# Kernel optimization log

Measured on AMD Instinct MI355X. Metric: run time of the kernel, lower is better.

The kernel has to match this reference:

```python
import jax, jax.numpy as jnp
import numpy as np

N, E = 50000, 640000
IN, HD, OUT, NCLS = 768, 128, 128, 2
H, C = 4, 32  # heads, per-head channels (HD/H = OUT/H = 32)
NEG_SLOPE = 0.2


def _glorot(key, shape):
    fan_in, fan_out = shape[0], shape[1]
    lim = jnp.sqrt(6.0 / (fan_in + fan_out))
    return jax.random.uniform(key, shape, jnp.float32, -lim, lim)


def setup_inputs() -> dict:
    key = jax.random.key(0)
    ks = jax.random.split(key, 24)
    x = jax.random.normal(ks[0], (1, N, IN), jnp.float32)
    edge_index = jax.random.randint(ks[1], (2, E), 0, N, jnp.int64)
    d = {"x": x, "edge_index": edge_index}
    ins = [IN, HD, HD, HD]
    for i in range(4):
        d[f"Wl{i+1}"] = _glorot(ks[2 + 5 * i], (ins[i], H * C))
        d[f"Wr{i+1}"] = _glorot(ks[3 + 5 * i], (ins[i], H * C))
        d[f"att{i+1}"] = _glorot(ks[4 + 5 * i], (H, C))
        d[f"b{i+1}"] = jnp.zeros((H * C,), jnp.float32)
    d["clfW"] = _glorot(ks[22], (OUT, NCLS))
    d["clfb"] = jnp.zeros((NCLS,), jnp.float32)
    return d


def _gatv2_layer(x, Wl, Wr, att, b, src, dst):
    # x: [N, F_in] -> out: [N, H*C]. GATv2: e = a^T LeakyReLU(xl_j + xr_i)
    xl = (x @ Wl).reshape(N, H, C)
    xr = (x @ Wr).reshape(N, H, C)
    h = xl[src] + xr[dst]                                   # [E', H, C] per-edge gather
    e = jnp.einsum('ehc,hc->eh', jax.nn.leaky_relu(h, NEG_SLOPE), att)
    m = jax.ops.segment_max(e, dst, num_segments=N)          # scatter-softmax (stable)
    a = jnp.exp(e - m[dst])
    s = jax.ops.segment_sum(a, dst, num_segments=N)
    alpha = a / (s[dst] + 1e-16)
    out = jax.ops.segment_sum(alpha[..., None] * xl[src], dst, num_segments=N)
    return out.reshape(N, H * C) + b


def reference(x, edge_index, Wl1, Wr1, att1, b1, Wl2, Wr2, att2, b2,
              Wl3, Wr3, att3, b3, Wl4, Wr4, att4, b4, clfW, clfb):
    xn = x.reshape(N, IN)  # torch.squeeze
    loops = jnp.arange(N, dtype=edge_index.dtype)  # PyG add_self_loops=True
    src = jnp.concatenate([edge_index[0], loops])
    dst = jnp.concatenate([edge_index[1], loops])
    h = jax.nn.relu(_gatv2_layer(xn, Wl1, Wr1, att1, b1, src, dst))
    h = jax.nn.relu(_gatv2_layer(h, Wl2, Wr2, att2, b2, src, dst))
    h = jax.nn.relu(_gatv2_layer(h, Wl3, Wr3, att3, b3, src, dst))
    h = _gatv2_layer(h, Wl4, Wr4, att4, b4, src, dst)        # [N, OUT]
    g = jnp.mean(h, axis=0, keepdims=True)                   # unsqueeze+mean over nodes -> [1, OUT]
    return g @ clfW + clfb                                   # [1, NCLS]
```

## Files before the change

kernel.cpp:

```cpp
#include <hip/hip_runtime.h>
#include <hip/hip_bf16.h>

#define NN 50000
#define EE 640000
#define HC 128
#define NB1 196

typedef short bf16x8 __attribute__((ext_vector_type(8)));
typedef float f32x4 __attribute__((ext_vector_type(4)));
typedef unsigned short u16;

__device__ __forceinline__ u16 f2b(float f) {
    unsigned u = __float_as_uint(f);
    unsigned r = u + 0x7FFFu + ((u >> 16) & 1u);
    return (u16)(r >> 16);
}
__device__ __forceinline__ float b2f(u16 h) {
    return __uint_as_float(((unsigned)h) << 16);
}

__device__ __forceinline__ void gload_lds16(const void* g, void* l) {
    __builtin_amdgcn_global_load_lds((const __attribute__((address_space(1))) void*)g,
                                     (__attribute__((address_space(3))) void*)l, 16, 0, 0);
}

__device__ __forceinline__ float red16(float x) {
    x += __int_as_float(__builtin_amdgcn_update_dpp(0, __float_as_int(x), 0xB1, 0xF, 0xF, true));
    x += __int_as_float(__builtin_amdgcn_update_dpp(0, __float_as_int(x), 0x4E, 0xF, 0xF, true));
    x += __int_as_float(__builtin_amdgcn_update_dpp(0, __float_as_int(x), 0x141, 0xF, 0xF, true));
    x += __int_as_float(__builtin_amdgcn_update_dpp(0, __float_as_int(x), 0x128, 0xF, 0xF, true));
    return x;
}


__global__ void k_count(const int* __restrict__ ei, int* __restrict__ cnt) {
    int e = blockIdx.x * blockDim.x + threadIdx.x;
    if (e < EE) atomicAdd(&cnt[ei[EE + e]], 1);
}

__global__ void k_bsum(const int* __restrict__ cnt, int* __restrict__ bsum) {
    __shared__ int sd[256];
    int b = blockIdx.x, t = threadIdx.x, i = b * 256 + t;
    sd[t] = (i < NN) ? cnt[i] + 1 : 0;
    __syncthreads();
    for (int o = 128; o; o >>= 1) { if (t < o) sd[t] += sd[t + o]; __syncthreads(); }
    if (!t) bsum[b] = sd[0];
}

__global__ void k_offs(const int* __restrict__ cnt_in, const int* __restrict__ bsum,
                       int* __restrict__ offs, int* __restrict__ cursor,
                       int* __restrict__ csr) {
    __shared__ int sb[256];
    __shared__ int sd[256];
    int b = blockIdx.x, t = threadIdx.x, i = b * 256 + t;
    sb[t] = (t < NB1) ? bsum[t] : 0;
    int v = (i < NN) ? cnt_in[i] + 1 : 0;
    sd[t] = v;
    __syncthreads();
    for (int o = 1; o < 256; o <<= 1) {
        int u1 = (t >= o) ? sd[t - o] : 0;
        int u2 = (t >= o) ? sb[t - o] : 0;
        __syncthreads();
        sd[t] += u1; sb[t] += u2;
        __syncthreads();
    }
    int bex = (b > 0) ? sb[b - 1] : 0;
    if (i < NN) {
        int o = bex + sd[t] - v;
        offs[i] = o;
        csr[o] = i;
        cursor[i] = o + 1;
    }
    if (b == NB1 - 1 && t == 0) offs[NN] = sb[NB1 - 1];
}

__global__ void k_fill(const int* __restrict__ ei, int* __restrict__ cursor,
                       int* __restrict__ csr) {
    int e = blockIdx.x * blockDim.x + threadIdx.x;
    if (e < EE) {
        int s = ei[e], d = ei[EE + e];
        int pos = atomicAdd(&cursor[d], 1);
        csr[pos] = s;
    }
}


#define WT_L0 196608
#define WT_LX 32768
#define WT_TOT (WT_L0 + 3 * WT_LX)

__global__ void k_castw_all(const float* __restrict__ Wl1, const float* __restrict__ Wr1,
                            const float* __restrict__ Wl2, const float* __restrict__ Wr2,
                            const float* __restrict__ Wl3, const float* __restrict__ Wr3,
                            const float* __restrict__ Wl4, const float* __restrict__ Wr4,
                            u16* __restrict__ WtAll) {
    int gid = blockIdx.x * 256 + threadIdx.x;
    if (gid >= WT_TOT) return;
    const float *Wl, *Wr;
    int idx, K, base;
    if (gid < WT_L0) { Wl = Wl1; Wr = Wr1; idx = gid; K = 768; base = 0; }
    else {
        int r = gid - WT_L0;
        int l = r >> 15; idx = r & (WT_LX - 1); K = 128; base = WT_L0 + l * WT_LX;
        if (l == 0)      { Wl = Wl2; Wr = Wr2; }
        else if (l == 1) { Wl = Wl3; Wr = Wr3; }
        else             { Wl = Wl4; Wr = Wr4; }
    }
    int c = idx / K, k = idx - c * K;
    float v = (c < 128) ? Wl[k * 128 + c] : Wr[k * 128 + (c - 128)];
    WtAll[base + idx] = f2b(v);
}


template<int K, bool F32A>
__global__ __launch_bounds__(512, 4)
void k_gemm(const void* __restrict__ Ag, const u16* __restrict__ Wt,
            u16* __restrict__ xb) {
    __shared__ __align__(16) u16 As[128 * 64];
    __shared__ __align__(16) u16 Bs[256 * 64];
    const int tid = threadIdx.x;
    const int wv = tid >> 6, ln = tid & 63;
    const int wr = wv >> 2, wc = wv & 3;
    const int m0 = blockIdx.x * 128;
    const int lrow = ln & 15, g = ln >> 4;

    f32x4 acc[4][4] = {};

    const float* Af = (const float*)Ag;
    const u16* Ab = (const u16*)Ag;
    const int arow = tid >> 2, aq = tid & 3;
    int arg = m0 + arow; if (arg >= NN) arg = 0;
    float4 ra0, ra1, ra2, ra3;

    if constexpr (F32A) {
        const float* src = Af + (size_t)arg * K + aq * 16;
        ra0 = *(const float4*)(src);
        ra1 = *(const float4*)(src + 4);
        ra2 = *(const float4*)(src + 8);
        ra3 = *(const float4*)(src + 12);
    }

    constexpr int NSTEP = K / 64;
    for (int ks = 0; ks < NSTEP; ++ks) {
        if constexpr (F32A) {
            const int s = arow & 7;
            bf16x8 v0, v1;
            v0[0] = (short)f2b(ra0.x); v0[1] = (short)f2b(ra0.y);
            v0[2] = (short)f2b(ra0.z); v0[3] = (short)f2b(ra0.w);
            v0[4] = (short)f2b(ra1.x); v0[5] = (short)f2b(ra1.y);
            v0[6] = (short)f2b(ra1.z); v0[7] = (short)f2b(ra1.w);
            v1[0] = (short)f2b(ra2.x); v1[1] = (short)f2b(ra2.y);
            v1[2] = (short)f2b(ra2.z); v1[3] = (short)f2b(ra2.w);
            v1[4] = (short)f2b(ra3.x); v1[5] = (short)f2b(ra3.y);
            v1[6] = (short)f2b(ra3.z); v1[7] = (short)f2b(ra3.w);
            *(bf16x8*)&As[arow * 64 + (((aq * 2) ^ s) * 8)] = v0;
            *(bf16x8*)&As[arow * 64 + (((aq * 2 + 1) ^ s) * 8)] = v1;
        } else {
            #pragma unroll
            for (int q = 0; q < 2; ++q) {
                int r8 = (wv * 2 + q) * 8;
                int row = r8 + (ln >> 3);
                int lc = (ln & 7) ^ (row & 7);
                int rg = m0 + row; if (rg >= NN) rg = 0;
                gload_lds16(Ab + (size_t)rg * K + ks * 64 + lc * 8, &As[r8 * 64]);
            }
        }
        #pragma unroll
        for (int q = 0; q < 4; ++q) {
            int r8 = (wv * 4 + q) * 8;
            int row = r8 + (ln >> 3);
            int lc = (ln & 7) ^ (row & 7);
            gload_lds16(Wt + (size_t)row * K + ks * 64 + lc * 8, &Bs[r8 * 64]);
        }
        __syncthreads();

        if constexpr (F32A) {
            if (ks + 1 < NSTEP) {
                const float* src = Af + (size_t)arg * K + (ks + 1) * 64 + aq * 16;
                ra0 = *(const float4*)(src);
                ra1 = *(const float4*)(src + 4);
                ra2 = *(const float4*)(src + 8);
                ra3 = *(const float4*)(src + 12);
            }
        }

        #pragma unroll
        for (int kk = 0; kk < 2; ++kk) {
            bf16x8 af[4], bfr[4];
            #pragma unroll
            for (int f = 0; f < 4; ++f) {
                int r = wr * 64 + f * 16 + lrow;
                af[f] = *(const bf16x8*)&As[r * 64 + (((kk * 4 + g) ^ (r & 7)) * 8)];
                int c = wc * 64 + f * 16 + lrow;
                bfr[f] = *(const bf16x8*)&Bs[c * 64 + (((kk * 4 + g) ^ (c & 7)) * 8)];
            }
            #pragma unroll
            for (int i = 0; i < 4; ++i)
                #pragma unroll
                for (int j = 0; j < 4; ++j)
                    acc[i][j] = __builtin_amdgcn_mfma_f32_16x16x32_bf16(af[i], bfr[j], acc[i][j], 0, 0, 0);
        }
        __syncthreads();
    }

    const int crow0 = m0 + wr * 64 + (g << 2);
    const int ccol0 = wc * 64 + lrow;
    #pragma unroll
    for (int i = 0; i < 4; ++i)
        #pragma unroll
        for (int rr = 0; rr < 4; ++rr) {
            int row = crow0 + i * 16 + rr;
            if (row < NN) {
                #pragma unroll
                for (int j = 0; j < 4; ++j)
                    xb[(size_t)row * 256 + ccol0 + j * 16] = f2b(acc[i][j][rr]);
            }
        }
}


__global__ __launch_bounds__(256)
void k_edge(const u16* __restrict__ xb, const float* __restrict__ att,
            const float* __restrict__ bias, const int* __restrict__ offs,
            const int* __restrict__ csr, u16* __restrict__ outb,
            float* __restrict__ outf, int relu) {
    int i = blockIdx.x * 4 + (threadIdx.x >> 6);
    if (i >= NN) return;
    int ln = threadIdx.x & 63;
    int ch0 = ((ln >> 4) << 5) + ((ln & 15) << 1);

    unsigned xr2 = *(const unsigned*)&xb[(size_t)i * 256 + 128 + ch0];
    float xri0 = b2f((u16)xr2), xri1 = b2f((u16)(xr2 >> 16));
    float2 atv = *(const float2*)&att[ch0];
    const float at0 = atv.x, at1 = atv.y;
    int beg = offs[i];
    int deg = offs[i + 1] - beg;

    float m0v = -3.0e38f, s0v = 0.f, p00 = 0.f, p01 = 0.f;
    float m1v = -3.0e38f, s1v = 0.f, p10 = 0.f, p11 = 0.f;
    float m2v = -3.0e38f, s2v = 0.f, p20 = 0.f, p21 = 0.f;
    float m3v = -3.0e38f, s3v = 0.f, p30 = 0.f, p31 = 0.f;

#define GATH(k, jj) unsigned w##k = *(const unsigned*)&xb[(size_t)(jj) * 256 + ch0];
#define UPD(k, M, S, A0, A1) { \
    float v0 = b2f((u16)w##k), v1 = b2f((u16)(w##k >> 16)); \
    float u0 = v0 + xri0; u0 = fmaxf(u0, 0.2f * u0); \
    float u1 = v1 + xri1; u1 = fmaxf(u1, 0.2f * u1); \
    float e = red16(u0 * at0 + u1 * at1); \
    float d = e - M; \
    float tt = __expf(-fabsf(d)); \
    bool ng = (d <= 0.f); \
    float c = ng ? 1.f : tt; \
    float ww = ng ? tt : 1.f; \
    M = ng ? M : e; \
    S = S * c + ww; A0 = A0 * c + ww * v0; A1 = A1 * c + ww * v1; }

    for (int base = 0; base < deg; base += 64) {
        int lim = deg - base; if (lim > 64) lim = 64;
        int idxv = (base + ln < deg) ? csr[beg + base + ln] : 0;
        int p = 0;
        for (; p + 4 <= lim; p += 4) {
            int j0 = __shfl(idxv, p);
            int j1 = __shfl(idxv, p + 1);
            int j2 = __shfl(idxv, p + 2);
            int j3 = __shfl(idxv, p + 3);
            GATH(0, j0) GATH(1, j1) GATH(2, j2) GATH(3, j3)
            UPD(0, m0v, s0v, p00, p01)
            UPD(1, m1v, s1v, p10, p11)
            UPD(2, m2v, s2v, p20, p21)
            UPD(3, m3v, s3v, p30, p31)
        }
        for (; p < lim; ++p) {
            int j0 = __shfl(idxv, p);
            GATH(4, j0)
            UPD(4, m0v, s0v, p00, p01)
        }
    }
#undef GATH
#undef UPD

    float mm = fmaxf(fmaxf(m0v, m1v), fmaxf(m2v, m3v));
    float c0 = __expf(m0v - mm), c1 = __expf(m1v - mm);
    float c2 = __expf(m2v - mm), c3 = __expf(m3v - mm);
    float s = s0v * c0 + s1v * c1 + s2v * c2 + s3v * c3 + 1e-16f;
    float inv = 1.f / s;
    float2 bv = *(const float2*)&bias[ch0];
    float o0 = (p00 * c0 + p10 * c1 + p20 * c2 + p30 * c3) * inv + bv.x;
    float o1 = (p01 * c0 + p11 * c1 + p21 * c2 + p31 * c3) * inv + bv.y;
    if (relu) { o0 = fmaxf(o0, 0.f); o1 = fmaxf(o1, 0.f); }
    if (outb) {
        unsigned pk = (unsigned)f2b(o0) | ((unsigned)f2b(o1) << 16);
        *(unsigned*)&outb[(size_t)i * HC + ch0] = pk;
    }
    if (outf) {
        *(float2*)&outf[(size_t)i * HC + ch0] = make_float2(o0, o1);
    }
}


__global__ __launch_bounds__(256)
void k_colsum(const float* __restrict__ h, float* __restrict__ gsum) {
    __shared__ float4 sd[8][32];
    int t = threadIdx.x;
    int c4 = t & 31, rl = t >> 5;
    float sx = 0.f, sy = 0.f, sz = 0.f, sw = 0.f;
    for (int r = blockIdx.x * 8 + rl; r < NN; r += 8 * gridDim.x) {
        float4 v = *(const float4*)&h[(size_t)r * HC + c4 * 4];
        sx += v.x; sy += v.y; sz += v.z; sw += v.w;
    }
    sd[rl][c4] = make_float4(sx, sy, sz, sw);
    __syncthreads();
    if (rl == 0) {
        float4 a = sd[0][c4];
        #pragma unroll
        for (int q = 1; q < 8; ++q) {
            float4 b = sd[q][c4];
            a.x += b.x; a.y += b.y; a.z += b.z; a.w += b.w;
        }
        atomicAdd(&gsum[c4 * 4 + 0], a.x);
        atomicAdd(&gsum[c4 * 4 + 1], a.y);
        atomicAdd(&gsum[c4 * 4 + 2], a.z);
        atomicAdd(&gsum[c4 * 4 + 3], a.w);
    }
}

__global__ void k_clf(const float* __restrict__ gsum, const float* __restrict__ W,
                      const float* __restrict__ bcls, float* __restrict__ out) {
    __shared__ float v[HC];
    int t = threadIdx.x;
    v[t] = gsum[t] * (1.f / (float)NN);
    __syncthreads();
    if (t < 2) {
        float r = 0.f;
        for (int k = 0; k < HC; ++k) r += v[k] * W[k * 2 + t];
        out[t] = r + bcls[t];
    }
}


extern "C" void kernel_launch(void* const* d_in, const int* in_sizes, int n_in,
                              void* d_out, int out_size, void* d_ws, size_t ws_size,
                              hipStream_t stream) {
    const float* x = (const float*)d_in[0];
    const int* ei = (const int*)d_in[1];
    const float *Wl[4], *Wr[4], *att[4], *bia[4];
    for (int l = 0; l < 4; ++l) {
        Wl[l] = (const float*)d_in[2 + 4 * l];
        Wr[l] = (const float*)d_in[3 + 4 * l];
        att[l] = (const float*)d_in[4 + 4 * l];
        bia[l] = (const float*)d_in[5 + 4 * l];
    }
    const float* clfW = (const float*)d_in[18];
    const float* clfb = (const float*)d_in[19];
    float* outp = (float*)d_out;

    char* w = (char*)d_ws;
    size_t o = 0;
    auto alloc = [&](size_t bytes) {
        char* p = w + o;
        o = (o + bytes + 255) & ~(size_t)255;
        return p;
    };
    int* cnt    = (int*)alloc((size_t)NN * 4);
    float* gsum = (float*)alloc(HC * 4);
    size_t zspan = o;
    int* offs  = (int*)alloc((size_t)(NN + 1) * 4);
    int* csr   = (int*)alloc((size_t)(EE + NN) * 4);
    int* bsum  = (int*)alloc((size_t)NB1 * 4);
    u16* WtAll = (u16*)alloc((size_t)WT_TOT * 2);
    u16* xb    = (u16*)alloc((size_t)NN * 256 * 2);
    u16* hb0   = (u16*)alloc((size_t)NN * HC * 2);
    u16* hb1   = (u16*)alloc((size_t)NN * HC * 2);
    float* hfin = (float*)alloc((size_t)NN * HC * 4);

    hipMemsetAsync(cnt, 0, zspan, stream);
    k_count<<<(EE + 255) / 256, 256, 0, stream>>>(ei, cnt);
    k_bsum<<<NB1, 256, 0, stream>>>(cnt, bsum);
    k_offs<<<NB1, 256, 0, stream>>>(cnt, bsum, offs, cnt, csr);
    k_fill<<<(EE + 255) / 256, 256, 0, stream>>>(ei, cnt, csr);
    k_castw_all<<<(WT_TOT + 255) / 256, 256, 0, stream>>>(
        Wl[0], Wr[0], Wl[1], Wr[1], Wl[2], Wr[2], Wl[3], Wr[3], WtAll);

    const int GB = (NN + 127) / 128;
    const u16* Wt_l[4] = {WtAll, WtAll + WT_L0, WtAll + WT_L0 + WT_LX,
                          WtAll + WT_L0 + 2 * WT_LX};
    const u16* hb_in = nullptr;
    u16* hbb[2] = {hb0, hb1};
    for (int l = 0; l < 4; ++l) {
        if (l == 0) k_gemm<768, true ><<<GB, 512, 0, stream>>>((const void*)x, Wt_l[0], xb);
        else        k_gemm<128, false><<<GB, 512, 0, stream>>>((const void*)hb_in, Wt_l[l], xb);
        u16* ob = (l < 3) ? hbb[l & 1] : nullptr;
        float* of = (l == 3) ? hfin : nullptr;
        k_edge<<<(NN + 3) / 4, 256, 0, stream>>>(xb, att[l], bia[l], offs, csr, ob, of,
                                                 (l < 3) ? 1 : 0);
        hb_in = ob;
    }

    k_colsum<<<504, 256, 0, stream>>>(hfin, gsum);
    k_clf<<<1, 128, 0, stream>>>(gsum, clfW, clfb, outp);
}
```

Baseline: 381.6 us.

## Switch to fp16 storage and MFMA, packed-half edge math with two nodes per wave

Replaces bf16 with fp16 throughout: weight cast, GEMM MFMA (f16 variant), and the projected feature buffer. The edge kernel now processes two destination nodes per wavefront, 32 lanes per node with 4 channels per lane. Leaky-ReLU and the attention dot product use packed half2 math and fdot2, and the per-head reduction needs one fewer cross-lane step (8 lanes instead of 16). Cheaper per-edge ALU work and wider gathers are bought with reduced fp16 range and precision, and with wasted iterations when the two nodes sharing a wave have unequal degree.

```diff
diff --git a/kernel.cpp b/kernel.cpp
--- a/kernel.cpp
+++ b/kernel.cpp
@@ -1,22 +1,23 @@
 #include <hip/hip_runtime.h>
 #include <hip/hip_bf16.h>
+#include <hip/hip_fp16.h>
 
 #define NN 50000
 #define EE 640000
 #define HC 128
 #define NB1 196
 
-typedef short bf16x8 __attribute__((ext_vector_type(8)));
+typedef _Float16 f16x8 __attribute__((ext_vector_type(8)));
+typedef _Float16 h2 __attribute__((ext_vector_type(2)));
 typedef float f32x4 __attribute__((ext_vector_type(4)));
 typedef unsigned short u16;
 
-__device__ __forceinline__ u16 f2b(float f) {
-    unsigned u = __float_as_uint(f);
-    unsigned r = u + 0x7FFFu + ((u >> 16) & 1u);
-    return (u16)(r >> 16);
-}
-__device__ __forceinline__ float b2f(u16 h) {
-    return __uint_as_float(((unsigned)h) << 16);
+__device__ __forceinline__ u16 f2h(float f) {
+    return __builtin_bit_cast(u16, (_Float16)f);
+}
+__device__ __forceinline__ h2 bch2(unsigned a) { return __builtin_bit_cast(h2, a); }
+__device__ __forceinline__ h2 habs2(h2 a) {
+    return __builtin_bit_cast(h2, __builtin_bit_cast(unsigned, a) & 0x7FFF7FFFu);
 }
 
 __device__ __forceinline__ void gload_lds16(const void* g, void* l) {
@@ -24,11 +25,10 @@
                                      (__attribute__((address_space(3))) void*)l, 16, 0, 0);
 }
 
-__device__ __forceinline__ float red16(float x) {
+__device__ __forceinline__ float red8(float x) {
     x += __int_as_float(__builtin_amdgcn_update_dpp(0, __float_as_int(x), 0xB1, 0xF, 0xF, true));
     x += __int_as_float(__builtin_amdgcn_update_dpp(0, __float_as_int(x), 0x4E, 0xF, 0xF, true));
-    x += __int_as_float(__builtin_amdgcn_update_dpp(0, __float_as_int(x), 0x141, 0xF, 0xF, true));
-    x += __int_as_float(__builtin_amdgcn_update_dpp(0, __float_as_int(x), 0x128, 0xF, 0xF, true));
+    x += __int_as_float(__builtin_amdgcn_ds_swizzle(__float_as_int(x), 0x101F));
     return x;
 }
 
@@ -108,7 +108,7 @@
     }
     int c = idx / K, k = idx - c * K;
     float v = (c < 128) ? Wl[k * 128 + c] : Wr[k * 128 + (c - 128)];
-    WtAll[base + idx] = f2b(v);
+    WtAll[base + idx] = f2h(v);
 }
 
 
@@ -144,17 +144,17 @@
     for (int ks = 0; ks < NSTEP; ++ks) {
         if constexpr (F32A) {
             const int s = arow & 7;
-            bf16x8 v0, v1;
-            v0[0] = (short)f2b(ra0.x); v0[1] = (short)f2b(ra0.y);
-            v0[2] = (short)f2b(ra0.z); v0[3] = (short)f2b(ra0.w);
-            v0[4] = (short)f2b(ra1.x); v0[5] = (short)f2b(ra1.y);
-            v0[6] = (short)f2b(ra1.z); v0[7] = (short)f2b(ra1.w);
-            v1[0] = (short)f2b(ra2.x); v1[1] = (short)f2b(ra2.y);
-            v1[2] = (short)f2b(ra2.z); v1[3] = (short)f2b(ra2.w);
-            v1[4] = (short)f2b(ra3.x); v1[5] = (short)f2b(ra3.y);
-            v1[6] = (short)f2b(ra3.z); v1[7] = (short)f2b(ra3.w);
-            *(bf16x8*)&As[arow * 64 + (((aq * 2) ^ s) * 8)] = v0;
-            *(bf16x8*)&As[arow * 64 + (((aq * 2 + 1) ^ s) * 8)] = v1;
+            f16x8 v0, v1;
+            v0[0] = (_Float16)ra0.x; v0[1] = (_Float16)ra0.y;
+            v0[2] = (_Float16)ra0.z; v0[3] = (_Float16)ra0.w;
+            v0[4] = (_Float16)ra1.x; v0[5] = (_Float16)ra1.y;
+            v0[6] = (_Float16)ra1.z; v0[7] = (_Float16)ra1.w;
+            v1[0] = (_Float16)ra2.x; v1[1] = (_Float16)ra2.y;
+            v1[2] = (_Float16)ra2.z; v1[3] = (_Float16)ra2.w;
+            v1[4] = (_Float16)ra3.x; v1[5] = (_Float16)ra3.y;
+            v1[6] = (_Float16)ra3.z; v1[7] = (_Float16)ra3.w;
+            *(f16x8*)&As[arow * 64 + (((aq * 2) ^ s) * 8)] = v0;
+            *(f16x8*)&As[arow * 64 + (((aq * 2 + 1) ^ s) * 8)] = v1;
         } else {
             #pragma unroll
             for (int q = 0; q < 2; ++q) {
@@ -186,19 +186,19 @@
 
         #pragma unroll
         for (int kk = 0; kk < 2; ++kk) {
-            bf16x8 af[4], bfr[4];
+            f16x8 af[4], bfr[4];
             #pragma unroll
             for (int f = 0; f < 4; ++f) {
                 int r = wr * 64 + f * 16 + lrow;
-                af[f] = *(const bf16x8*)&As[r * 64 + (((kk * 4 + g) ^ (r & 7)) * 8)];
+                af[f] = *(const f16x8*)&As[r * 64 + (((kk * 4 + g) ^ (r & 7)) * 8)];
                 int c = wc * 64 + f * 16 + lrow;
-                bfr[f] = *(const bf16x8*)&Bs[c * 64 + (((kk * 4 + g) ^ (c & 7)) * 8)];
+                bfr[f] = *(const f16x8*)&Bs[c * 64 + (((kk * 4 + g) ^ (c & 7)) * 8)];
             }
             #pragma unroll
             for (int i = 0; i < 4; ++i)
                 #pragma unroll
                 for (int j = 0; j < 4; ++j)
-                    acc[i][j] = __builtin_amdgcn_mfma_f32_16x16x32_bf16(af[i], bfr[j], acc[i][j], 0, 0, 0);
+                    acc[i][j] = __builtin_amdgcn_mfma_f32_16x16x32_f16(af[i], bfr[j], acc[i][j], 0, 0, 0);
         }
         __syncthreads();
     }
@@ -213,7 +213,7 @@
             if (row < NN) {
                 #pragma unroll
                 for (int j = 0; j < 4; ++j)
-                    xb[(size_t)row * 256 + ccol0 + j * 16] = f2b(acc[i][j][rr]);
+                    xb[(size_t)row * 256 + ccol0 + j * 16] = f2h(acc[i][j][rr]);
             }
         }
 }
@@ -224,56 +224,63 @@
             const float* __restrict__ bias, const int* __restrict__ offs,
             const int* __restrict__ csr, u16* __restrict__ outb,
             float* __restrict__ outf, int relu) {
-    int i = blockIdx.x * 4 + (threadIdx.x >> 6);
-    if (i >= NN) return;
-    int ln = threadIdx.x & 63;
-    int ch0 = ((ln >> 4) << 5) + ((ln & 15) << 1);
-
-    unsigned xr2 = *(const unsigned*)&xb[(size_t)i * 256 + 128 + ch0];
-    float xri0 = b2f((u16)xr2), xri1 = b2f((u16)(xr2 >> 16));
-    float2 atv = *(const float2*)&att[ch0];
-    const float at0 = atv.x, at1 = atv.y;
+    const int wv = threadIdx.x >> 6;
+    const int ln = threadIdx.x & 63;
+    const int half = ln >> 5, lh = ln & 31;
+    const int i = blockIdx.x * 8 + wv * 2 + half;
+    const int c4 = lh * 4;
+
+    uint2 xrw = *(const uint2*)&xb[(size_t)i * 256 + 128 + c4];
+    const h2 xr01 = bch2(xrw.x), xr23 = bch2(xrw.y);
+    float4 av = *(const float4*)&att[c4];
+    const h2 at01 = {(_Float16)av.x, (_Float16)av.y};
+    const h2 at23 = {(_Float16)av.z, (_Float16)av.w};
+    const h2 C06 = {(_Float16)0.6f, (_Float16)0.6f};
+    const h2 C04 = {(_Float16)0.4f, (_Float16)0.4f};
+
     int beg = offs[i];
     int deg = offs[i + 1] - beg;
-
-    float m0v = -3.0e38f, s0v = 0.f, p00 = 0.f, p01 = 0.f;
-    float m1v = -3.0e38f, s1v = 0.f, p10 = 0.f, p11 = 0.f;
-    float m2v = -3.0e38f, s2v = 0.f, p20 = 0.f, p21 = 0.f;
-    float m3v = -3.0e38f, s3v = 0.f, p30 = 0.f, p31 = 0.f;
-
-#define GATH(k, jj) unsigned w##k = *(const unsigned*)&xb[(size_t)(jj) * 256 + ch0];
-#define UPD(k, M, S, A0, A1) { \
-    float v0 = b2f((u16)w##k), v1 = b2f((u16)(w##k >> 16)); \
-    float u0 = v0 + xri0; u0 = fmaxf(u0, 0.2f * u0); \
-    float u1 = v1 + xri1; u1 = fmaxf(u1, 0.2f * u1); \
-    float e = red16(u0 * at0 + u1 * at1); \
+    int degO = __shfl_xor(deg, 32);
+    int degM = (deg > degO) ? deg : degO;
+
+    float m0v = -3.0e38f, s0v = 0.f, a00 = 0.f, a01 = 0.f, a02 = 0.f, a03 = 0.f;
+    float m1v = -3.0e38f, s1v = 0.f, a10 = 0.f, a11 = 0.f, a12 = 0.f, a13 = 0.f;
+    float m2v = -3.0e38f, s2v = 0.f, a20 = 0.f, a21 = 0.f, a22 = 0.f, a23 = 0.f;
+    float m3v = -3.0e38f, s3v = 0.f, a30 = 0.f, a31 = 0.f, a32 = 0.f, a33 = 0.f;
+
+#define GATH(k, jj) uint2 w##k = *(const uint2*)&xb[(size_t)(jj) * 256 + c4];
+#define UPD(k, M, S, A0, A1, A2, A3, ok) { \
+    h2 v01 = bch2(w##k.x), v23 = bch2(w##k.y); \
+    h2 u01 = v01 + xr01, u23 = v23 + xr23; \
+    h2 l01 = u01 * C06 + habs2(u01) * C04; \
+    h2 l23 = u23 * C06 + habs2(u23) * C04; \
+    float e = __builtin_amdgcn_fdot2(l01, at01, \
+              __builtin_amdgcn_fdot2(l23, at23, 0.f, false), false); \
+    e = red8(e); \
     float d = e - M; \
     float tt = __expf(-fabsf(d)); \
-    bool ng = (d <= 0.f); \
+    bool ng = (d <= 0.f) || (!(ok)); \
     float c = ng ? 1.f : tt; \
-    float ww = ng ? tt : 1.f; \
+    float ww = (ok) ? (ng ? tt : 1.f) : 0.f; \
     M = ng ? M : e; \
-    S = S * c + ww; A0 = A0 * c + ww * v0; A1 = A1 * c + ww * v1; }
-
-    for (int base = 0; base < deg; base += 64) {
-        int lim = deg - base; if (lim > 64) lim = 64;
-        int idxv = (base + ln < deg) ? csr[beg + base + ln] : 0;
-        int p = 0;
-        for (; p + 4 <= lim; p += 4) {
-            int j0 = __shfl(idxv, p);
-            int j1 = __shfl(idxv, p + 1);
-            int j2 = __shfl(idxv, p + 2);
-            int j3 = __shfl(idxv, p + 3);
+    S = S * c + ww; \
+    A0 = A0 * c + ww * (float)v01[0]; A1 = A1 * c + ww * (float)v01[1]; \
+    A2 = A2 * c + ww * (float)v23[0]; A3 = A3 * c + ww * (float)v23[1]; }
+
+    for (int base = 0; base < degM; base += 32) {
+        int idxv = (base + lh < deg) ? csr[beg + base + lh] : i;
+        int lim = degM - base; if (lim > 32) lim = 32;
+        int myl = deg - base;
+        for (int p = 0; p < lim; p += 4) {
+            int j0 = __shfl(idxv, p + 0, 32);
+            int j1 = __shfl(idxv, p + 1, 32);
+            int j2 = __shfl(idxv, p + 2, 32);
+            int j3 = __shfl(idxv, p + 3, 32);
             GATH(0, j0) GATH(1, j1) GATH(2, j2) GATH(3, j3)
-            UPD(0, m0v, s0v, p00, p01)
-            UPD(1, m1v, s1v, p10, p11)
-            UPD(2, m2v, s2v, p20, p21)
-            UPD(3, m3v, s3v, p30, p31)
-        }
-        for (; p < lim; ++p) {
-            int j0 = __shfl(idxv, p);
-            GATH(4, j0)
-            UPD(4, m0v, s0v, p00, p01)
+            UPD(0, m0v, s0v, a00, a01, a02, a03, (p + 0 < myl))
+            UPD(1, m1v, s1v, a10, a11, a12, a13, (p + 1 < myl))
+            UPD(2, m2v, s2v, a20, a21, a22, a23, (p + 2 < myl))
+            UPD(3, m3v, s3v, a30, a31, a32, a33, (p + 3 < myl))
         }
     }
 #undef GATH
@@ -284,16 +291,23 @@
     float c2 = __expf(m2v - mm), c3 = __expf(m3v - mm);
     float s = s0v * c0 + s1v * c1 + s2v * c2 + s3v * c3 + 1e-16f;
     float inv = 1.f / s;
-    float2 bv = *(const float2*)&bias[ch0];
-    float o0 = (p00 * c0 + p10 * c1 + p20 * c2 + p30 * c3) * inv + bv.x;
-    float o1 = (p01 * c0 + p11 * c1 + p21 * c2 + p31 * c3) * inv + bv.y;
-    if (relu) { o0 = fmaxf(o0, 0.f); o1 = fmaxf(o1, 0.f); }
+    float4 bv = *(const float4*)&bias[c4];
+    float o0 = (a00 * c0 + a10 * c1 + a20 * c2 + a30 * c3) * inv + bv.x;
+    float o1 = (a01 * c0 + a11 * c1 + a21 * c2 + a31 * c3) * inv + bv.y;
+    float o2 = (a02 * c0 + a12 * c1 + a22 * c2 + a32 * c3) * inv + bv.z;
+    float o3 = (a03 * c0 + a13 * c1 + a23 * c2 + a33 * c3) * inv + bv.w;
+    if (relu) {
+        o0 = fmaxf(o0, 0.f); o1 = fmaxf(o1, 0.f);
+        o2 = fmaxf(o2, 0.f); o3 = fmaxf(o3, 0.f);
+    }
     if (outb) {
-        unsigned pk = (unsigned)f2b(o0) | ((unsigned)f2b(o1) << 16);
-        *(unsigned*)&outb[(size_t)i * HC + ch0] = pk;
+        uint2 pk;
+        pk.x = (unsigned)f2h(o0) | ((unsigned)f2h(o1) << 16);
+        pk.y = (unsigned)f2h(o2) | ((unsigned)f2h(o3) << 16);
+        *(uint2*)&outb[(size_t)i * HC + c4] = pk;
     }
     if (outf) {
-        *(float2*)&outf[(size_t)i * HC + ch0] = make_float2(o0, o1);
+        *(float4*)&outf[(size_t)i * HC + c4] = make_float4(o0, o1, o2, o3);
     }
 }
 
@@ -391,8 +405,8 @@
         else        k_gemm<128, false><<<GB, 512, 0, stream>>>((const void*)hb_in, Wt_l[l], xb);
         u16* ob = (l < 3) ? hbb[l & 1] : nullptr;
         float* of = (l == 3) ? hfin : nullptr;
-        k_edge<<<(NN + 3) / 4, 256, 0, stream>>>(xb, att[l], bia[l], offs, csr, ob, of,
-                                                 (l < 3) ? 1 : 0);
+        k_edge<<<NN / 8, 256, 0, stream>>>(xb, att[l], bia[l], offs, csr, ob, of,
+                                           (l < 3) ? 1 : 0);
         hb_in = ob;
     }
 
```

New measurement: 364.8 us. -4.4%, faster.
